# Optimization experiments

Measured on AMD Instinct MI355X. Metric: run time of the kernel, lower is better.

The kernel has to match this reference:

```python
import jax, jax.numpy as jnp
import numpy as np

D_MODEL = 1024
NUM_HEADS = 16
DEPTH = D_MODEL // NUM_HEADS


def setup_inputs() -> dict:
    key = jax.random.key(0)
    ks = jax.random.split(key, 6)
    B, S = 2, 2048
    scale = 1.0 / np.sqrt(D_MODEL)
    return {
        "q": jax.random.normal(ks[0], (B, S, D_MODEL), jnp.float32),
        "k": jax.random.normal(ks[1], (B, S, D_MODEL), jnp.float32),
        "v": jax.random.normal(ks[2], (B, S, D_MODEL), jnp.float32),
        "wq": jax.random.normal(ks[3], (D_MODEL, D_MODEL), jnp.float32) * scale,
        "wk": jax.random.normal(ks[4], (D_MODEL, D_MODEL), jnp.float32) * scale,
        "wv": jax.random.normal(ks[5], (D_MODEL, D_MODEL), jnp.float32) * scale,
    }


def reference(q, k, v, wq, wk, wv):
    B, S, _ = q.shape
    # Linear projections (nn.Linear: x @ W.T), then split heads -> [B,H,S,depth]
    def split(x):
        return x.reshape(B, -1, NUM_HEADS, DEPTH).transpose(0, 2, 1, 3)
    Q = split(q @ wq.T)
    K = split(k @ wk.T)
    V = split(v @ wv.T)
    scores = jnp.einsum("bhqd,bhkd->bhqk", Q, K) / np.sqrt(DEPTH).astype(np.float32)
    attn = jax.nn.softmax(scores, axis=-1)
    out = jnp.einsum("bhqk,bhkd->bhqd", attn, V)
    # merge heads; note: original forward never applies self.dense
    return out.transpose(0, 2, 1, 3).reshape(B, S, D_MODEL)
```

## Files before the change

kernel.cpp:

```cpp
#include <hip/hip_runtime.h>
#include <hip/hip_bf16.h>
#include <stdint.h>

#define B_SZ 2
#define S_LEN 2048
#define DM 1024
#define NH 16
#define DEPTH 64
#define M_ROWS (B_SZ * S_LEN)
#define SCALE_Q 0.1803368801111144f

typedef __attribute__((ext_vector_type(8))) short bf16x8;
typedef __attribute__((ext_vector_type(4))) float f32x4;
typedef __attribute__((ext_vector_type(16))) float f32x16;

__device__ __forceinline__ unsigned short f2bf(float x) {
    union { float f; unsigned u; } a; a.f = x;
    unsigned r = a.u + 0x7FFF + ((a.u >> 16) & 1);
    return (unsigned short)(r >> 16);
}

__device__ __forceinline__ bf16x8 u4_to_bf8(uint4 u) {
    union { uint4 a; bf16x8 b; } c; c.a = u; return c.b;
}

__device__ __forceinline__ unsigned cvtpk_bf16(float lo, float hi) {
    unsigned r;
    asm("v_cvt_pk_bf16_f32 %0, %1, %2" : "=v"(r) : "v"(lo), "v"(hi));
    return r;
}

__device__ __forceinline__ void permswap32(unsigned &a, unsigned &b) {
    auto r = __builtin_amdgcn_permlane32_swap(a, b, false, false);
    a = r[0]; b = r[1];
}

__device__ __forceinline__ void async_ld16(const unsigned short* g, void* l) {
    __builtin_amdgcn_global_load_lds(
        (const __attribute__((address_space(1))) void*)g,
        (__attribute__((address_space(3))) void*)l,
        16, 0, 0);
}


__global__ __launch_bounds__(256)
void convert_kernel(const float* __restrict__ q, const float* __restrict__ k,
                    const float* __restrict__ v, const float* __restrict__ wq,
                    const float* __restrict__ wk, const float* __restrict__ wv,
                    unsigned short* __restrict__ dst) {
    const int z = blockIdx.y;
    const float* src = (z == 0) ? q : (z == 1) ? k : (z == 2) ? v
                     : (z == 3) ? wq : (z == 4) ? wk : wv;
    const size_t n4  = (z < 3) ? ((size_t)M_ROWS * DM / 4) : ((size_t)DM * DM / 4);
    const size_t off = (z < 3) ? ((size_t)z * M_ROWS * DM)
                               : ((size_t)3 * M_ROWS * DM + (size_t)(z - 3) * DM * DM);
    unsigned short* d = dst + off;
    const size_t stride = (size_t)gridDim.x * blockDim.x;
    for (size_t i = (size_t)blockIdx.x * blockDim.x + threadIdx.x; i < n4; i += stride) {
        float4 x = ((const float4*)src)[i];
        ushort4 p;
        p.x = f2bf(x.x); p.y = f2bf(x.y); p.z = f2bf(x.z); p.w = f2bf(x.w);
        ((ushort4*)d)[i] = p;
    }
}

__global__ __launch_bounds__(256)
void proj_gemm3_kernel(const unsigned short* __restrict__ Xall,
                       const unsigned short* __restrict__ Wall,
                       unsigned short* __restrict__ Call) {
    __shared__ unsigned short As[128 * 64];
    __shared__ unsigned short Bs[128 * 64];

    const int z = blockIdx.z;
    const unsigned short* X = Xall + (size_t)z * M_ROWS * DM;
    const unsigned short* W = Wall + (size_t)z * DM * DM;
    unsigned short* C = Call + (size_t)z * M_ROWS * DM;

    const int tid  = threadIdx.x;
    const int wave = tid >> 6;
    const int lane = tid & 63;
    const int l32  = lane & 31;
    const int s    = lane >> 5;
    const int m0 = blockIdx.x * 128;
    const int n0 = blockIdx.y * 128;
    const int wm = (wave >> 1) * 64;
    const int wn = (wave & 1) * 64;

    const int r8 = lane >> 3;
    const int sc = (lane & 7) ^ r8;

    f32x16 acc[2][2];
#pragma unroll
    for (int mi = 0; mi < 2; ++mi)
#pragma unroll
        for (int ni = 0; ni < 2; ++ni)
#pragma unroll
            for (int r = 0; r < 16; ++r) acc[mi][ni][r] = 0.f;

    for (int k0 = 0; k0 < DM; k0 += 64) {
#pragma unroll
        for (int i = 0; i < 4; ++i) {
            const int r = i * 32 + wave * 8 + r8;
            async_ld16(X + (size_t)(m0 + r) * DM + k0 + sc * 8,
                       (char*)As + i * 4096 + wave * 1024);
            async_ld16(W + (size_t)(n0 + r) * DM + k0 + sc * 8,
                       (char*)Bs + i * 4096 + wave * 1024);
        }
        __syncthreads();

#pragma unroll
        for (int ch = 0; ch < 4; ++ch) {
            bf16x8 af[2], bfr[2];
#pragma unroll
            for (int mi = 0; mi < 2; ++mi) {
                const int row = wm + mi * 32 + l32;
                af[mi] = *(const bf16x8*)&As[row * 64 + (((2 * ch + s) ^ (row & 7)) * 8)];
            }
#pragma unroll
            for (int ni = 0; ni < 2; ++ni) {
                const int row = wn + ni * 32 + l32;
                bfr[ni] = *(const bf16x8*)&Bs[row * 64 + (((2 * ch + s) ^ (row & 7)) * 8)];
            }
#pragma unroll
            for (int mi = 0; mi < 2; ++mi)
#pragma unroll
                for (int ni = 0; ni < 2; ++ni)
                    acc[mi][ni] = __builtin_amdgcn_mfma_f32_32x32x16_bf16(
                        af[mi], bfr[ni], acc[mi][ni], 0, 0, 0);
        }
        __syncthreads();
    }

    const float scale = (z == 0) ? SCALE_Q : 1.0f;
#pragma unroll
    for (int mi = 0; mi < 2; ++mi)
#pragma unroll
        for (int ni = 0; ni < 2; ++ni)
#pragma unroll
            for (int r = 0; r < 16; ++r) {
                const int row = m0 + wm + mi * 32 + (r & 3) + 8 * (r >> 2) + 4 * s;
                const int col = n0 + wn + ni * 32 + l32;
                C[(size_t)row * DM + col] = f2bf(acc[mi][ni][r] * scale);
            }
}

__global__ __launch_bounds__(256)
void vtrans_kernel(const unsigned short* __restrict__ Vp,
                   unsigned short* __restrict__ Vt) {
    __shared__ unsigned short Ls[64 * 72];
    const int tr = blockIdx.x;
    const int h  = blockIdx.y;
    const int tid = threadIdx.x;

#pragma unroll
    for (int i = 0; i < 2; ++i) {
        const int id = i * 256 + tid;
        const int r = id >> 3, c = id & 7;
        bf16x8 v8 = *(const bf16x8*)&Vp[(size_t)(tr * 64 + r) * DM + h * 64 + c * 8];
        *(bf16x8*)&Ls[r * 72 + ((c ^ (r & 7)) * 8)] = v8;
    }
    __syncthreads();

    const int b = tr >> 5;
    const int col0 = (tr & 31) * 64;
#pragma unroll
    for (int i = 0; i < 2; ++i) {
        const int id = i * 256 + tid;
        const int d = id >> 3, c2 = id & 7;
        unsigned short tmp[8];
#pragma unroll
        for (int j = 0; j < 8; ++j) {
            const int t = c2 * 8 + j;
            tmp[j] = Ls[t * 72 + (((d >> 3) ^ (t & 7)) * 8) + (d & 7)];
        }
        *(bf16x8*)&Vt[(size_t)((b * NH + h) * DEPTH + d) * S_LEN + col0 + c2 * 8] =
            *(const bf16x8*)tmp;
    }
}

__global__ __launch_bounds__(128, 2)
void attn8_kernel(const unsigned short* __restrict__ Qp,
                  const unsigned short* __restrict__ Kp,
                  const unsigned short* __restrict__ Vt,
                  float* __restrict__ out,
                  float* __restrict__ Op1,
                  float* __restrict__ lp) {
    __shared__ __align__(16) char smem[32768];
    unsigned short* Ks = (unsigned short*)smem;
    unsigned short* Vs = (unsigned short*)(smem + 16384);

    const int tid  = threadIdx.x;
    const int w    = tid >> 6;
    const int lane = tid & 63;
    const int l32  = lane & 31;
    const int s    = lane >> 5;
    const int r8   = lane >> 3;
    const int sc   = (lane & 7) ^ r8;

    const int q0 = blockIdx.x * 128 + w * 64;
    const int h  = blockIdx.y;
    const int z  = blockIdx.z;
    const int b     = z >> 1;
    const int split = z & 1;
    const int tbase = split * 1024;

    const unsigned short* Kg = Kp + (size_t)(b * S_LEN + tbase) * DM + h * DEPTH;
    const unsigned short* Vg = Vt + (size_t)((b * NH + h) * DEPTH) * S_LEN + tbase;
    float* obase = split ? Op1 : out;
    float* lbase = lp + (size_t)split * M_ROWS * NH;

    bf16x8 qf[2][4];
#pragma unroll
    for (int nq = 0; nq < 2; ++nq) {
        const unsigned short* p =
            Qp + (size_t)(b * S_LEN + q0 + nq * 32 + l32) * DM + h * DEPTH;
#pragma unroll
        for (int ch = 0; ch < 4; ++ch)
            qf[nq][ch] = *(const bf16x8*)(p + ch * 16 + s * 8);
    }

    f32x16 oacc[2][2];
    float lacc[2] = {0.f, 0.f};
#pragma unroll
    for (int db = 0; db < 2; ++db)
#pragma unroll
        for (int nq = 0; nq < 2; ++nq)
#pragma unroll
            for (int r = 0; r < 16; ++r) oacc[db][nq][r] = 0.f;

#pragma unroll
    for (int i = 0; i < 4; ++i)
        async_ld16(Kg + (size_t)(w * 32 + i * 8 + r8) * DM + sc * 8,
                   (char*)smem + w * 4096 + i * 1024);
#pragma unroll
    for (int i = 0; i < 4; ++i)
        async_ld16(Vg + (size_t)(w * 32 + i * 8 + r8) * S_LEN + sc * 8,
                   (char*)smem + 16384 + w * 4096 + i * 1024);

    for (int it = 0; it < 16; ++it) {
        const int cb = it & 1;

        asm volatile("s_waitcnt vmcnt(0) lgkmcnt(0)" ::: "memory");
        __syncthreads();

        if (it < 15) {
            const int tn = (it + 1) * 64;
            char* kd = (char*)smem + (cb ^ 1) * 8192 + w * 4096;
            char* vd = (char*)smem + 16384 + (cb ^ 1) * 8192 + w * 4096;
#pragma unroll
            for (int i = 0; i < 4; ++i)
                async_ld16(Kg + (size_t)(tn + w * 32 + i * 8 + r8) * DM + sc * 8,
                           kd + i * 1024);
#pragma unroll
            for (int i = 0; i < 4; ++i)
                async_ld16(Vg + (size_t)(w * 32 + i * 8 + r8) * S_LEN + tn + sc * 8,
                           vd + i * 1024);
        }

        const unsigned short* Kb = Ks + cb * 4096;
        const unsigned short* Vb = Vs + cb * 4096;

#pragma unroll
        for (int th = 0; th < 2; ++th) {
            const unsigned short* Kh = Kb + th * 2048;
            const int vcb = th * 4;

            f32x16 s0, s1;
#pragma unroll
            for (int r = 0; r < 16; ++r) { s0[r] = 0.f; s1[r] = 0.f; }
            __builtin_amdgcn_s_setprio(1);
#pragma unroll
            for (int ch = 0; ch < 4; ++ch) {
                bf16x8 kf = *(const bf16x8*)
                    &Kh[l32 * 64 + (((2 * ch + s) ^ (l32 & 7)) * 8)];
                s0 = __builtin_amdgcn_mfma_f32_32x32x16_bf16(kf, qf[0][ch], s0, 0, 0, 0);
                s1 = __builtin_amdgcn_mfma_f32_32x32x16_bf16(kf, qf[1][ch], s1, 0, 0, 0);
            }
            __builtin_amdgcn_s_setprio(0);

            unsigned pw[2][8];
#pragma unroll
            for (int nq = 0; nq < 2; ++nq) {
                float p[16];
#pragma unroll
                for (int r = 0; r < 16; ++r)
                    p[r] = __builtin_amdgcn_exp2f(nq ? s1[r] : s0[r]);
                lacc[nq] += ((p[0] + p[1]) + (p[2] + p[3]))
                          + ((p[4] + p[5]) + (p[6] + p[7]))
                          + ((p[8] + p[9]) + (p[10] + p[11]))
                          + ((p[12] + p[13]) + (p[14] + p[15]));
                unsigned a0 = cvtpk_bf16(p[0],  p[1]);
                unsigned b0 = cvtpk_bf16(p[4],  p[5]);
                unsigned a1 = cvtpk_bf16(p[2],  p[3]);
                unsigned b1 = cvtpk_bf16(p[6],  p[7]);
                unsigned a2 = cvtpk_bf16(p[8],  p[9]);
                unsigned b2 = cvtpk_bf16(p[12], p[13]);
                unsigned a3 = cvtpk_bf16(p[10], p[11]);
                unsigned b3 = cvtpk_bf16(p[14], p[15]);
                permswap32(a0, b0);
                permswap32(a1, b1);
                permswap32(a2, b2);
                permswap32(a3, b3);
                pw[nq][0] = a0; pw[nq][1] = a1; pw[nq][2] = b0; pw[nq][3] = b1;
                pw[nq][4] = a2; pw[nq][5] = a3; pw[nq][6] = b2; pw[nq][7] = b3;
            }

#pragma unroll
            for (int ch = 0; ch < 2; ++ch) {
                bf16x8 pf[2];
#pragma unroll
                for (int nq = 0; nq < 2; ++nq) {
                    uint4 pu;
                    pu.x = pw[nq][ch * 4 + 0];
                    pu.y = pw[nq][ch * 4 + 1];
                    pu.z = pw[nq][ch * 4 + 2];
                    pu.w = pw[nq][ch * 4 + 3];
                    pf[nq] = u4_to_bf8(pu);
                }
                __builtin_amdgcn_s_setprio(1);
#pragma unroll
                for (int db = 0; db < 2; ++db) {
                    const int drow = db * 32 + l32;
                    bf16x8 vf = *(const bf16x8*)
                        &Vb[drow * 64 + (((vcb + 2 * ch + s) ^ (l32 & 7)) * 8)];
                    oacc[db][0] = __builtin_amdgcn_mfma_f32_32x32x16_bf16(
                        vf, pf[0], oacc[db][0], 0, 0, 0);
                    oacc[db][1] = __builtin_amdgcn_mfma_f32_32x32x16_bf16(
                        vf, pf[1], oacc[db][1], 0, 0, 0);
                }
                __builtin_amdgcn_s_setprio(0);
            }
        }
    }

    asm volatile("s_waitcnt vmcnt(0)" ::: "memory");

    const float l0 = lacc[0] + __shfl_xor(lacc[0], 32, 64);
    const float l1 = lacc[1] + __shfl_xor(lacc[1], 32, 64);
    if (s == 0) {
        lbase[(size_t)(b * S_LEN + q0 + l32) * NH + h]      = l0;
        lbase[(size_t)(b * S_LEN + q0 + 32 + l32) * NH + h] = l1;
    }

    __syncthreads();
    float* Of = (float*)(smem + w * 4608);
#pragma unroll
    for (int c = 0; c < 4; ++c) {
        const int nq = c >> 1;
        if ((l32 >> 4) == (c & 1)) {
            const int qh = l32 & 15;
#pragma unroll
            for (int db = 0; db < 2; ++db)
#pragma unroll
                for (int m = 0; m < 4; ++m) {
                    float4 v;
                    v.x = oacc[db][nq][4 * m + 0];
                    v.y = oacc[db][nq][4 * m + 1];
                    v.z = oacc[db][nq][4 * m + 2];
                    v.w = oacc[db][nq][4 * m + 3];
                    *(float4*)&Of[qh * 68 + db * 32 + 8 * m + 4 * s] = v;
                }
        }
        asm volatile("" ::: "memory");
#pragma unroll
        for (int i = 0; i < 4; ++i) {
            const int row = i * 4 + (lane >> 4);
            const int c4 = lane & 15;
            float4 v = *(const float4*)&Of[row * 68 + c4 * 4];
            *(float4*)&obase[(size_t)(b * S_LEN + q0 + c * 16 + row) * DM
                             + h * DEPTH + c4 * 4] = v;
        }
        asm volatile("" ::: "memory");
    }
}

__global__ __launch_bounds__(256)
void combine_kernel(float* __restrict__ out, const float* __restrict__ Op1,
                    const float* __restrict__ lp) {
    const int i4 = blockIdx.x * 256 + threadIdx.x;
    const int row = i4 >> 8;
    const int c4  = i4 & 255;
    const int h   = c4 >> 4;
    const float l = lp[row * NH + h] + lp[M_ROWS * NH + row * NH + h];
    const float inv = 1.0f / l;
    float4 a = ((const float4*)out)[i4];
    float4 bq = ((const float4*)Op1)[i4];
    a.x = (a.x + bq.x) * inv;
    a.y = (a.y + bq.y) * inv;
    a.z = (a.z + bq.z) * inv;
    a.w = (a.w + bq.w) * inv;
    ((float4*)out)[i4] = a;
}

#define LDK 72

__global__ __launch_bounds__(256)
void proj_gemm_kernel(const float* __restrict__ q, const float* __restrict__ k,
                      const float* __restrict__ v, const float* __restrict__ wq,
                      const float* __restrict__ wk, const float* __restrict__ wv,
                      unsigned short* __restrict__ Qp, unsigned short* __restrict__ Kp,
                      unsigned short* __restrict__ Vp) {
    __shared__ unsigned short As[128 * LDK];
    __shared__ unsigned short Bs[128 * LDK];

    const int z = blockIdx.z;
    const float* __restrict__ X = (z == 0) ? q : (z == 1) ? k : v;
    const float* __restrict__ W = (z == 0) ? wq : (z == 1) ? wk : wv;
    unsigned short* __restrict__ C = (z == 0) ? Qp : (z == 1) ? Kp : Vp;

    const int tid  = threadIdx.x;
    const int wave = tid >> 6;
    const int lane = tid & 63;
    const int quad = lane >> 4;
    const int l16  = lane & 15;
    const int m0 = blockIdx.x * 128;
    const int n0 = blockIdx.y * 128;
    const int wm = (wave >> 1) * 64;
    const int wn = (wave & 1) * 64;

    f32x4 acc[4][4];
#pragma unroll
    for (int mt = 0; mt < 4; ++mt)
#pragma unroll
        for (int nt = 0; nt < 4; ++nt)
            acc[mt][nt] = (f32x4){0.f, 0.f, 0.f, 0.f};

    for (int k0 = 0; k0 < DM; k0 += 64) {
#pragma unroll
        for (int vv = 0; vv < 8; ++vv) {
            int vecid = tid + 256 * vv;
            int r  = vecid >> 4;
            int c4 = vecid & 15;
            const float4 xa = *(const float4*)&X[(size_t)(m0 + r) * DM + k0 + c4 * 4];
            ushort4 pa;
            pa.x = f2bf(xa.x); pa.y = f2bf(xa.y); pa.z = f2bf(xa.z); pa.w = f2bf(xa.w);
            *(ushort4*)&As[r * LDK + c4 * 4] = pa;
            const float4 xb = *(const float4*)&W[(size_t)(n0 + r) * DM + k0 + c4 * 4];
            ushort4 pb;
            pb.x = f2bf(xb.x); pb.y = f2bf(xb.y); pb.z = f2bf(xb.z); pb.w = f2bf(xb.w);
            *(ushort4*)&Bs[r * LDK + c4 * 4] = pb;
        }
        __syncthreads();

#pragma unroll
        for (int kc = 0; kc < 2; ++kc) {
            bf16x8 af[4], bfr[4];
#pragma unroll
            for (int mt = 0; mt < 4; ++mt)
                af[mt] = *(const bf16x8*)&As[(wm + mt * 16 + l16) * LDK + kc * 32 + quad * 8];
#pragma unroll
            for (int nt = 0; nt < 4; ++nt)
                bfr[nt] = *(const bf16x8*)&Bs[(wn + nt * 16 + l16) * LDK + kc * 32 + quad * 8];
#pragma unroll
            for (int mt = 0; mt < 4; ++mt)
#pragma unroll
                for (int nt = 0; nt < 4; ++nt)
                    acc[mt][nt] = __builtin_amdgcn_mfma_f32_16x16x32_bf16(
                        af[mt], bfr[nt], acc[mt][nt], 0, 0, 0);
        }
        __syncthreads();
    }

#pragma unroll
    for (int mt = 0; mt < 4; ++mt)
#pragma unroll
        for (int nt = 0; nt < 4; ++nt)
#pragma unroll
            for (int r = 0; r < 4; ++r) {
                int row = m0 + wm + mt * 16 + quad * 4 + r;
                int col = n0 + wn + nt * 16 + l16;
                C[(size_t)row * DM + col] = f2bf(acc[mt][nt][r]);
            }
}

__global__ __launch_bounds__(256)
void attn_kernel(const unsigned short* __restrict__ Qp,
                 const unsigned short* __restrict__ Kp,
                 const unsigned short* __restrict__ Vp,
                 float* __restrict__ out) {
    __shared__ unsigned short Ks[64 * LDK];
    __shared__ unsigned short Vtl[64 * LDK];
    __shared__ unsigned short Ps[4 * 16 * LDK];

    const int tid  = threadIdx.x;
    const int wave = tid >> 6;
    const int lane = tid & 63;
    const int quad = lane >> 4;
    const int l16  = lane & 15;
    const int q0 = blockIdx.x * 64;
    const int h  = blockIdx.y;
    const int b  = blockIdx.z;
    const int wbase = wave * 16 * LDK;

    bf16x8 qf[2];
    {
        size_t row = (size_t)b * S_LEN + q0 + wave * 16 + l16;
        const unsigned short* p = Qp + row * DM + h * DEPTH;
        qf[0] = *(const bf16x8*)(p + quad * 8);
        qf[1] = *(const bf16x8*)(p + 32 + quad * 8);
    }

    float m_i[4], l_i[4];
    f32x4 accO[4];
#pragma unroll
    for (int r = 0; r < 4; ++r) { m_i[r] = -1e30f; l_i[r] = 0.f; }
#pragma unroll
    for (int f = 0; f < 4; ++f) accO[f] = (f32x4){0.f, 0.f, 0.f, 0.f};

    for (int t0 = 0; t0 < S_LEN; t0 += 64) {
#pragma unroll
        for (int vv = 0; vv < 2; ++vv) {
            int vecid = tid + 256 * vv;
            int r  = vecid >> 3;
            int cv = vecid & 7;
            size_t grow = (size_t)(b * S_LEN + t0 + r) * DM + h * DEPTH + cv * 8;
            *(bf16x8*)&Ks[r * LDK + cv * 8] = *(const bf16x8*)(Kp + grow);
            bf16x8 vvv = *(const bf16x8*)(Vp + grow);
#pragma unroll
            for (int j = 0; j < 8; ++j)
                Vtl[(cv * 8 + j) * LDK + r] = ((const unsigned short*)&vvv)[j];
        }
        __syncthreads();

        f32x4 sc4[4];
#pragma unroll
        for (int nt = 0; nt < 4; ++nt) {
            f32x4 a = (f32x4){0.f, 0.f, 0.f, 0.f};
            bf16x8 kf0 = *(const bf16x8*)&Ks[(nt * 16 + l16) * LDK + quad * 8];
            bf16x8 kf1 = *(const bf16x8*)&Ks[(nt * 16 + l16) * LDK + 32 + quad * 8];
            a = __builtin_amdgcn_mfma_f32_16x16x32_bf16(qf[0], kf0, a, 0, 0, 0);
            a = __builtin_amdgcn_mfma_f32_16x16x32_bf16(qf[1], kf1, a, 0, 0, 0);
            sc4[nt] = a;
        }
#pragma unroll
        for (int nt = 0; nt < 4; ++nt)
#pragma unroll
            for (int r = 0; r < 4; ++r) sc4[nt][r] *= 0.125f;

#pragma unroll
        for (int r = 0; r < 4; ++r) {
            float mx = fmaxf(fmaxf(sc4[0][r], sc4[1][r]), fmaxf(sc4[2][r], sc4[3][r]));
#pragma unroll
            for (int off = 1; off < 16; off <<= 1)
                mx = fmaxf(mx, __shfl_xor(mx, off, 64));
            float mnew = fmaxf(m_i[r], mx);
            float alpha = __expf(m_i[r] - mnew);
            float rs = 0.f;
#pragma unroll
            for (int nt = 0; nt < 4; ++nt) {
                float p = __expf(sc4[nt][r] - mnew);
                sc4[nt][r] = p;
                rs += p;
            }
#pragma unroll
            for (int off = 1; off < 16; off <<= 1)
                rs += __shfl_xor(rs, off, 64);
            l_i[r] = l_i[r] * alpha + rs;
            m_i[r] = mnew;
#pragma unroll
            for (int f = 0; f < 4; ++f) accO[f][r] *= alpha;
        }

#pragma unroll
        for (int nt = 0; nt < 4; ++nt)
#pragma unroll
            for (int r = 0; r < 4; ++r)
                Ps[wbase + (quad * 4 + r) * LDK + nt * 16 + l16] = f2bf(sc4[nt][r]);
        __syncthreads();

        bf16x8 pf0 = *(const bf16x8*)&Ps[wbase + l16 * LDK + quad * 8];
        bf16x8 pf1 = *(const bf16x8*)&Ps[wbase + l16 * LDK + 32 + quad * 8];
#pragma unroll
        for (int f = 0; f < 4; ++f) {
            bf16x8 vf0 = *(const bf16x8*)&Vtl[(f * 16 + l16) * LDK + quad * 8];
            bf16x8 vf1 = *(const bf16x8*)&Vtl[(f * 16 + l16) * LDK + 32 + quad * 8];
            accO[f] = __builtin_amdgcn_mfma_f32_16x16x32_bf16(pf0, vf0, accO[f], 0, 0, 0);
            accO[f] = __builtin_amdgcn_mfma_f32_16x16x32_bf16(pf1, vf1, accO[f], 0, 0, 0);
        }
        __syncthreads();
    }

#pragma unroll
    for (int f = 0; f < 4; ++f)
#pragma unroll
        for (int r = 0; r < 4; ++r) {
            size_t row = (size_t)b * S_LEN + q0 + wave * 16 + quad * 4 + r;
            out[row * DM + h * DEPTH + f * 16 + l16] = accO[f][r] / l_i[r];
        }
}

extern "C" void kernel_launch(void* const* d_in, const int* in_sizes, int n_in,
                              void* d_out, int out_size, void* d_ws, size_t ws_size,
                              hipStream_t stream) {
    const float* q  = (const float*)d_in[0];
    const float* k  = (const float*)d_in[1];
    const float* v  = (const float*)d_in[2];
    const float* wq = (const float*)d_in[3];
    const float* wk = (const float*)d_in[4];
    const float* wv = (const float*)d_in[5];
    float* out = (float*)d_out;

    unsigned short* ws = (unsigned short*)d_ws;
    const size_t NPROJ = (size_t)M_ROWS * DM;
    const size_t NW    = (size_t)DM * DM;

    const size_t need = (3 * NPROJ + 3 * NW + 3 * NPROJ) * sizeof(unsigned short);

    if (ws_size >= need) {
        unsigned short* Xbf = ws;
        unsigned short* Wbf = ws + 3 * NPROJ;
        unsigned short* Cp  = ws + 3 * NPROJ + 3 * NW;
        unsigned short* Qp  = Cp;
        unsigned short* Kp  = Cp + NPROJ;
        unsigned short* Vp  = Cp + 2 * NPROJ;
        unsigned short* Vt  = ws;
        float*          Op1 = (float*)(ws + NPROJ);
        float*          lp  = (float*)(ws + 3 * NPROJ);

        convert_kernel<<<dim3(256, 6), 256, 0, stream>>>(q, k, v, wq, wk, wv, Xbf);
        proj_gemm3_kernel<<<dim3(M_ROWS / 128, DM / 128, 3), 256, 0, stream>>>(Xbf, Wbf, Cp);
        vtrans_kernel<<<dim3(M_ROWS / 64, NH), 256, 0, stream>>>(Vp, Vt);
        attn8_kernel<<<dim3(S_LEN / 128, NH, 4), 128, 0, stream>>>(
            Qp, Kp, Vt, out, Op1, lp);
        combine_kernel<<<dim3(M_ROWS * DM / 4 / 256), 256, 0, stream>>>(out, Op1, lp);
    } else {
        unsigned short* Qp = ws;
        unsigned short* Kp = ws + NPROJ;
        unsigned short* Vp = ws + 2 * NPROJ;
        proj_gemm_kernel<<<dim3(M_ROWS / 128, DM / 128, 3), 256, 0, stream>>>(
            q, k, v, wq, wk, wv, Qp, Kp, Vp);
        attn_kernel<<<dim3(S_LEN / 64, NH, B_SZ), 256, 0, stream>>>(Qp, Kp, Vp, out);
    }
}
```

Baseline: 198.1 us.

## Load K/V fragments directly from global into registers, dropping LDS staging

Replaces the shared-memory double-buffered async K/V tile pipeline in the attention kernel with per-wave direct global loads into register fragments. Loads for the next 32-key half-tile are issued before the current half-step computes. This removes the block barriers and LDS traffic, and shrinks shared memory to only the output staging buffer. The cost is that each wave now fetches K and V separately, so global and L2 traffic roughly doubles. The reads are also narrower, 16B per lane on strided rows, and register pressure rises.

```diff
diff --git a/kernel.cpp b/kernel.cpp
--- a/kernel.cpp
+++ b/kernel.cpp
@@ -178,6 +178,85 @@
     }
 }
 
+__device__ __forceinline__ void attn_half_step(
+    const bf16x8* kf, const bf16x8* vf, const bf16x8 (&qf)[2][4],
+    f32x16 (&oacc)[2][2], float* lacc) {
+    f32x16 s0, s1;
+#pragma unroll
+    for (int r = 0; r < 16; ++r) { s0[r] = 0.f; s1[r] = 0.f; }
+    __builtin_amdgcn_s_setprio(1);
+#pragma unroll
+    for (int ch = 0; ch < 4; ++ch) {
+        s0 = __builtin_amdgcn_mfma_f32_32x32x16_bf16(kf[ch], qf[0][ch], s0, 0, 0, 0);
+        s1 = __builtin_amdgcn_mfma_f32_32x32x16_bf16(kf[ch], qf[1][ch], s1, 0, 0, 0);
+    }
+    __builtin_amdgcn_s_setprio(0);
+
+    unsigned pw[2][8];
+#pragma unroll
+    for (int nq = 0; nq < 2; ++nq) {
+        float p[16];
+#pragma unroll
+        for (int r = 0; r < 16; ++r)
+            p[r] = __builtin_amdgcn_exp2f(nq ? s1[r] : s0[r]);
+        lacc[nq] += ((p[0] + p[1]) + (p[2] + p[3]))
+                  + ((p[4] + p[5]) + (p[6] + p[7]))
+                  + ((p[8] + p[9]) + (p[10] + p[11]))
+                  + ((p[12] + p[13]) + (p[14] + p[15]));
+        unsigned a0 = cvtpk_bf16(p[0],  p[1]);
+        unsigned b0 = cvtpk_bf16(p[4],  p[5]);
+        unsigned a1 = cvtpk_bf16(p[2],  p[3]);
+        unsigned b1 = cvtpk_bf16(p[6],  p[7]);
+        unsigned a2 = cvtpk_bf16(p[8],  p[9]);
+        unsigned b2 = cvtpk_bf16(p[12], p[13]);
+        unsigned a3 = cvtpk_bf16(p[10], p[11]);
+        unsigned b3 = cvtpk_bf16(p[14], p[15]);
+        permswap32(a0, b0);
+        permswap32(a1, b1);
+        permswap32(a2, b2);
+        permswap32(a3, b3);
+        pw[nq][0] = a0; pw[nq][1] = a1; pw[nq][2] = b0; pw[nq][3] = b1;
+        pw[nq][4] = a2; pw[nq][5] = a3; pw[nq][6] = b2; pw[nq][7] = b3;
+    }
+
+#pragma unroll
+    for (int ch = 0; ch < 2; ++ch) {
+        bf16x8 pf[2];
+#pragma unroll
+        for (int nq = 0; nq < 2; ++nq) {
+            uint4 pu;
+            pu.x = pw[nq][ch * 4 + 0];
+            pu.y = pw[nq][ch * 4 + 1];
+            pu.z = pw[nq][ch * 4 + 2];
+            pu.w = pw[nq][ch * 4 + 3];
+            pf[nq] = u4_to_bf8(pu);
+        }
+        __builtin_amdgcn_s_setprio(1);
+#pragma unroll
+        for (int db = 0; db < 2; ++db) {
+            oacc[db][0] = __builtin_amdgcn_mfma_f32_32x32x16_bf16(
+                vf[ch * 2 + db], pf[0], oacc[db][0], 0, 0, 0);
+            oacc[db][1] = __builtin_amdgcn_mfma_f32_32x32x16_bf16(
+                vf[ch * 2 + db], pf[1], oacc[db][1], 0, 0, 0);
+        }
+        __builtin_amdgcn_s_setprio(0);
+    }
+}
+
+__device__ __forceinline__ void load_kf(bf16x8* kf, const unsigned short* kp) {
+#pragma unroll
+    for (int ch = 0; ch < 4; ++ch)
+        kf[ch] = *(const bf16x8*)(kp + ch * 16);
+}
+__device__ __forceinline__ void load_vf(bf16x8* vf, const unsigned short* vp0,
+                                        const unsigned short* vp1) {
+#pragma unroll
+    for (int ch = 0; ch < 2; ++ch) {
+        vf[ch * 2 + 0] = *(const bf16x8*)(vp0 + ch * 16);
+        vf[ch * 2 + 1] = *(const bf16x8*)(vp1 + ch * 16);
+    }
+}
+
 __global__ __launch_bounds__(128, 2)
 void attn8_kernel(const unsigned short* __restrict__ Qp,
                   const unsigned short* __restrict__ Kp,
@@ -185,17 +264,13 @@
                   float* __restrict__ out,
                   float* __restrict__ Op1,
                   float* __restrict__ lp) {
-    __shared__ __align__(16) char smem[32768];
-    unsigned short* Ks = (unsigned short*)smem;
-    unsigned short* Vs = (unsigned short*)(smem + 16384);
+    __shared__ __align__(16) float Of_s[2][1088];
 
     const int tid  = threadIdx.x;
     const int w    = tid >> 6;
     const int lane = tid & 63;
     const int l32  = lane & 31;
     const int s    = lane >> 5;
-    const int r8   = lane >> 3;
-    const int sc   = (lane & 7) ^ r8;
 
     const int q0 = blockIdx.x * 128 + w * 64;
     const int h  = blockIdx.y;
@@ -228,112 +303,27 @@
 #pragma unroll
             for (int r = 0; r < 16; ++r) oacc[db][nq][r] = 0.f;
 
-#pragma unroll
-    for (int i = 0; i < 4; ++i)
-        async_ld16(Kg + (size_t)(w * 32 + i * 8 + r8) * DM + sc * 8,
-                   (char*)smem + w * 4096 + i * 1024);
-#pragma unroll
-    for (int i = 0; i < 4; ++i)
-        async_ld16(Vg + (size_t)(w * 32 + i * 8 + r8) * S_LEN + sc * 8,
-                   (char*)smem + 16384 + w * 4096 + i * 1024);
-
-    for (int it = 0; it < 16; ++it) {
-        const int cb = it & 1;
-
-        asm volatile("s_waitcnt vmcnt(0) lgkmcnt(0)" ::: "memory");
-        __syncthreads();
-
-        if (it < 15) {
-            const int tn = (it + 1) * 64;
-            char* kd = (char*)smem + (cb ^ 1) * 8192 + w * 4096;
-            char* vd = (char*)smem + 16384 + (cb ^ 1) * 8192 + w * 4096;
-#pragma unroll
-            for (int i = 0; i < 4; ++i)
-                async_ld16(Kg + (size_t)(tn + w * 32 + i * 8 + r8) * DM + sc * 8,
-                           kd + i * 1024);
-#pragma unroll
-            for (int i = 0; i < 4; ++i)
-                async_ld16(Vg + (size_t)(w * 32 + i * 8 + r8) * S_LEN + tn + sc * 8,
-                           vd + i * 1024);
-        }
-
-        const unsigned short* Kb = Ks + cb * 4096;
-        const unsigned short* Vb = Vs + cb * 4096;
-
-#pragma unroll
-        for (int th = 0; th < 2; ++th) {
-            const unsigned short* Kh = Kb + th * 2048;
-            const int vcb = th * 4;
-
-            f32x16 s0, s1;
-#pragma unroll
-            for (int r = 0; r < 16; ++r) { s0[r] = 0.f; s1[r] = 0.f; }
-            __builtin_amdgcn_s_setprio(1);
-#pragma unroll
-            for (int ch = 0; ch < 4; ++ch) {
-                bf16x8 kf = *(const bf16x8*)
-                    &Kh[l32 * 64 + (((2 * ch + s) ^ (l32 & 7)) * 8)];
-                s0 = __builtin_amdgcn_mfma_f32_32x32x16_bf16(kf, qf[0][ch], s0, 0, 0, 0);
-                s1 = __builtin_amdgcn_mfma_f32_32x32x16_bf16(kf, qf[1][ch], s1, 0, 0, 0);
-            }
-            __builtin_amdgcn_s_setprio(0);
-
-            unsigned pw[2][8];
-#pragma unroll
-            for (int nq = 0; nq < 2; ++nq) {
-                float p[16];
-#pragma unroll
-                for (int r = 0; r < 16; ++r)
-                    p[r] = __builtin_amdgcn_exp2f(nq ? s1[r] : s0[r]);
-                lacc[nq] += ((p[0] + p[1]) + (p[2] + p[3]))
-                          + ((p[4] + p[5]) + (p[6] + p[7]))
-                          + ((p[8] + p[9]) + (p[10] + p[11]))
-                          + ((p[12] + p[13]) + (p[14] + p[15]));
-                unsigned a0 = cvtpk_bf16(p[0],  p[1]);
-                unsigned b0 = cvtpk_bf16(p[4],  p[5]);
-                unsigned a1 = cvtpk_bf16(p[2],  p[3]);
-                unsigned b1 = cvtpk_bf16(p[6],  p[7]);
-                unsigned a2 = cvtpk_bf16(p[8],  p[9]);
-                unsigned b2 = cvtpk_bf16(p[12], p[13]);
-                unsigned a3 = cvtpk_bf16(p[10], p[11]);
-                unsigned b3 = cvtpk_bf16(p[14], p[15]);
-                permswap32(a0, b0);
-                permswap32(a1, b1);
-                permswap32(a2, b2);
-                permswap32(a3, b3);
-                pw[nq][0] = a0; pw[nq][1] = a1; pw[nq][2] = b0; pw[nq][3] = b1;
-                pw[nq][4] = a2; pw[nq][5] = a3; pw[nq][6] = b2; pw[nq][7] = b3;
-            }
-
-#pragma unroll
-            for (int ch = 0; ch < 2; ++ch) {
-                bf16x8 pf[2];
-#pragma unroll
-                for (int nq = 0; nq < 2; ++nq) {
-                    uint4 pu;
-                    pu.x = pw[nq][ch * 4 + 0];
-                    pu.y = pw[nq][ch * 4 + 1];
-                    pu.z = pw[nq][ch * 4 + 2];
-                    pu.w = pw[nq][ch * 4 + 3];
-                    pf[nq] = u4_to_bf8(pu);
-                }
-                __builtin_amdgcn_s_setprio(1);
-#pragma unroll
-                for (int db = 0; db < 2; ++db) {
-                    const int drow = db * 32 + l32;
-                    bf16x8 vf = *(const bf16x8*)
-                        &Vb[drow * 64 + (((vcb + 2 * ch + s) ^ (l32 & 7)) * 8)];
-                    oacc[db][0] = __builtin_amdgcn_mfma_f32_32x32x16_bf16(
-                        vf, pf[0], oacc[db][0], 0, 0, 0);
-                    oacc[db][1] = __builtin_amdgcn_mfma_f32_32x32x16_bf16(
-                        vf, pf[1], oacc[db][1], 0, 0, 0);
-                }
-                __builtin_amdgcn_s_setprio(0);
-            }
-        }
-    }
-
-    asm volatile("s_waitcnt vmcnt(0)" ::: "memory");
+    const unsigned short* kp  = Kg + (size_t)l32 * DM + s * 8;
+    const unsigned short* vp0 = Vg + (size_t)l32 * S_LEN + s * 8;
+    const unsigned short* vp1 = Vg + (size_t)(32 + l32) * S_LEN + s * 8;
+
+    bf16x8 kA[4], vA[4], kB[4], vB[4];
+    load_kf(kA, kp);
+    load_vf(vA, vp0, vp1);
+
+    for (int hp = 0; hp < 16; ++hp) {
+        load_kf(kB, kp + 32 * DM);
+        load_vf(vB, vp0 + 32, vp1 + 32);
+        attn_half_step(kA, vA, qf, oacc, lacc);
+        if (hp < 15) {
+            load_kf(kA, kp + 64 * DM);
+            load_vf(vA, vp0 + 64, vp1 + 64);
+        }
+        attn_half_step(kB, vB, qf, oacc, lacc);
+        kp  += 64 * DM;
+        vp0 += 64;
+        vp1 += 64;
+    }
 
     const float l0 = lacc[0] + __shfl_xor(lacc[0], 32, 64);
     const float l1 = lacc[1] + __shfl_xor(lacc[1], 32, 64);
@@ -342,8 +332,7 @@
         lbase[(size_t)(b * S_LEN + q0 + 32 + l32) * NH + h] = l1;
     }
 
-    __syncthreads();
-    float* Of = (float*)(smem + w * 4608);
+    float* Of = Of_s[w];
 #pragma unroll
     for (int c = 0; c < 4; ++c) {
         const int nq = c >> 1;
```

Result: slower. 213.2 us (+7.6%).

## Split attention block across four waves with 32 query rows each

Applied to the files above, without the earlier changes.

The attention kernel now runs 256 threads (four waves) per block instead of two. Each wave handles 32 query rows instead of 64, and the K/V tile loads are spread across four waves. This cuts per-wave register use (one score accumulator and two output accumulators) so more waves can be resident. In exchange, each K/V fragment read from shared memory feeds fewer MFMAs, which lowers data reuse per wave.

```diff
diff --git a/kernel.cpp b/kernel.cpp
--- a/kernel.cpp
+++ b/kernel.cpp
@@ -178,7 +178,7 @@
     }
 }
 
-__global__ __launch_bounds__(128, 2)
+__global__ __launch_bounds__(256, 4)
 void attn8_kernel(const unsigned short* __restrict__ Qp,
                   const unsigned short* __restrict__ Kp,
                   const unsigned short* __restrict__ Vt,
@@ -197,7 +197,7 @@
     const int r8   = lane >> 3;
     const int sc   = (lane & 7) ^ r8;
 
-    const int q0 = blockIdx.x * 128 + w * 64;
+    const int q0 = blockIdx.x * 128 + w * 32;
     const int h  = blockIdx.y;
     const int z  = blockIdx.z;
     const int b     = z >> 1;
@@ -209,33 +209,29 @@
     float* obase = split ? Op1 : out;
     float* lbase = lp + (size_t)split * M_ROWS * NH;
 
-    bf16x8 qf[2][4];
-#pragma unroll
-    for (int nq = 0; nq < 2; ++nq) {
+    bf16x8 qf[4];
+    {
         const unsigned short* p =
-            Qp + (size_t)(b * S_LEN + q0 + nq * 32 + l32) * DM + h * DEPTH;
+            Qp + (size_t)(b * S_LEN + q0 + l32) * DM + h * DEPTH;
 #pragma unroll
         for (int ch = 0; ch < 4; ++ch)
-            qf[nq][ch] = *(const bf16x8*)(p + ch * 16 + s * 8);
-    }
-
-    f32x16 oacc[2][2];
-    float lacc[2] = {0.f, 0.f};
+            qf[ch] = *(const bf16x8*)(p + ch * 16 + s * 8);
+    }
+
+    f32x16 oacc[2];
+    float lacc = 0.f;
 #pragma unroll
     for (int db = 0; db < 2; ++db)
 #pragma unroll
-        for (int nq = 0; nq < 2; ++nq)
-#pragma unroll
-            for (int r = 0; r < 16; ++r) oacc[db][nq][r] = 0.f;
-
-#pragma unroll
-    for (int i = 0; i < 4; ++i)
-        async_ld16(Kg + (size_t)(w * 32 + i * 8 + r8) * DM + sc * 8,
-                   (char*)smem + w * 4096 + i * 1024);
-#pragma unroll
-    for (int i = 0; i < 4; ++i)
-        async_ld16(Vg + (size_t)(w * 32 + i * 8 + r8) * S_LEN + sc * 8,
-                   (char*)smem + 16384 + w * 4096 + i * 1024);
+        for (int r = 0; r < 16; ++r) oacc[db][r] = 0.f;
+
+#pragma unroll
+    for (int i = 0; i < 2; ++i) {
+        async_ld16(Kg + (size_t)(w * 16 + i * 8 + r8) * DM + sc * 8,
+                   (char*)smem + w * 2048 + i * 1024);
+        async_ld16(Vg + (size_t)(w * 16 + i * 8 + r8) * S_LEN + sc * 8,
+                   (char*)smem + 16384 + w * 2048 + i * 1024);
+    }
 
     for (int it = 0; it < 16; ++it) {
         const int cb = it & 1;
@@ -245,16 +241,15 @@
 
         if (it < 15) {
             const int tn = (it + 1) * 64;
-            char* kd = (char*)smem + (cb ^ 1) * 8192 + w * 4096;
-            char* vd = (char*)smem + 16384 + (cb ^ 1) * 8192 + w * 4096;
-#pragma unroll
-            for (int i = 0; i < 4; ++i)
-                async_ld16(Kg + (size_t)(tn + w * 32 + i * 8 + r8) * DM + sc * 8,
+            char* kd = (char*)smem + (cb ^ 1) * 8192 + w * 2048;
+            char* vd = (char*)smem + 16384 + (cb ^ 1) * 8192 + w * 2048;
+#pragma unroll
+            for (int i = 0; i < 2; ++i) {
+                async_ld16(Kg + (size_t)(tn + w * 16 + i * 8 + r8) * DM + sc * 8,
                            kd + i * 1024);
-#pragma unroll
-            for (int i = 0; i < 4; ++i)
-                async_ld16(Vg + (size_t)(w * 32 + i * 8 + r8) * S_LEN + tn + sc * 8,
+                async_ld16(Vg + (size_t)(w * 16 + i * 8 + r8) * S_LEN + tn + sc * 8,
                            vd + i * 1024);
+            }
         }
 
         const unsigned short* Kb = Ks + cb * 4096;
@@ -265,68 +260,58 @@
             const unsigned short* Kh = Kb + th * 2048;
             const int vcb = th * 4;
 
-            f32x16 s0, s1;
-#pragma unroll
-            for (int r = 0; r < 16; ++r) { s0[r] = 0.f; s1[r] = 0.f; }
+            f32x16 s0;
+#pragma unroll
+            for (int r = 0; r < 16; ++r) s0[r] = 0.f;
             __builtin_amdgcn_s_setprio(1);
 #pragma unroll
             for (int ch = 0; ch < 4; ++ch) {
                 bf16x8 kf = *(const bf16x8*)
                     &Kh[l32 * 64 + (((2 * ch + s) ^ (l32 & 7)) * 8)];
-                s0 = __builtin_amdgcn_mfma_f32_32x32x16_bf16(kf, qf[0][ch], s0, 0, 0, 0);
-                s1 = __builtin_amdgcn_mfma_f32_32x32x16_bf16(kf, qf[1][ch], s1, 0, 0, 0);
+                s0 = __builtin_amdgcn_mfma_f32_32x32x16_bf16(kf, qf[ch], s0, 0, 0, 0);
             }
             __builtin_amdgcn_s_setprio(0);
 
-            unsigned pw[2][8];
-#pragma unroll
-            for (int nq = 0; nq < 2; ++nq) {
-                float p[16];
-#pragma unroll
-                for (int r = 0; r < 16; ++r)
-                    p[r] = __builtin_amdgcn_exp2f(nq ? s1[r] : s0[r]);
-                lacc[nq] += ((p[0] + p[1]) + (p[2] + p[3]))
-                          + ((p[4] + p[5]) + (p[6] + p[7]))
-                          + ((p[8] + p[9]) + (p[10] + p[11]))
-                          + ((p[12] + p[13]) + (p[14] + p[15]));
-                unsigned a0 = cvtpk_bf16(p[0],  p[1]);
-                unsigned b0 = cvtpk_bf16(p[4],  p[5]);
-                unsigned a1 = cvtpk_bf16(p[2],  p[3]);
-                unsigned b1 = cvtpk_bf16(p[6],  p[7]);
-                unsigned a2 = cvtpk_bf16(p[8],  p[9]);
-                unsigned b2 = cvtpk_bf16(p[12], p[13]);
-                unsigned a3 = cvtpk_bf16(p[10], p[11]);
-                unsigned b3 = cvtpk_bf16(p[14], p[15]);
-                permswap32(a0, b0);
-                permswap32(a1, b1);
-                permswap32(a2, b2);
-                permswap32(a3, b3);
-                pw[nq][0] = a0; pw[nq][1] = a1; pw[nq][2] = b0; pw[nq][3] = b1;
-                pw[nq][4] = a2; pw[nq][5] = a3; pw[nq][6] = b2; pw[nq][7] = b3;
-            }
+            float p[16];
+#pragma unroll
+            for (int r = 0; r < 16; ++r)
+                p[r] = __builtin_amdgcn_exp2f(s0[r]);
+            lacc += ((p[0] + p[1]) + (p[2] + p[3]))
+                  + ((p[4] + p[5]) + (p[6] + p[7]))
+                  + ((p[8] + p[9]) + (p[10] + p[11]))
+                  + ((p[12] + p[13]) + (p[14] + p[15]));
+            unsigned a0 = cvtpk_bf16(p[0],  p[1]);
+            unsigned b0 = cvtpk_bf16(p[4],  p[5]);
+            unsigned a1 = cvtpk_bf16(p[2],  p[3]);
+            unsigned b1 = cvtpk_bf16(p[6],  p[7]);
+            unsigned a2 = cvtpk_bf16(p[8],  p[9]);
+            unsigned b2 = cvtpk_bf16(p[12], p[13]);
+            unsigned a3 = cvtpk_bf16(p[10], p[11]);
+            unsigned b3 = cvtpk_bf16(p[14], p[15]);
+            permswap32(a0, b0);
+            permswap32(a1, b1);
+            permswap32(a2, b2);
+            permswap32(a3, b3);
+            unsigned pw[8];
+            pw[0] = a0; pw[1] = a1; pw[2] = b0; pw[3] = b1;
+            pw[4] = a2; pw[5] = a3; pw[6] = b2; pw[7] = b3;
 
 #pragma unroll
             for (int ch = 0; ch < 2; ++ch) {
-                bf16x8 pf[2];
-#pragma unroll
-                for (int nq = 0; nq < 2; ++nq) {
-                    uint4 pu;
-                    pu.x = pw[nq][ch * 4 + 0];
-                    pu.y = pw[nq][ch * 4 + 1];
-                    pu.z = pw[nq][ch * 4 + 2];
-                    pu.w = pw[nq][ch * 4 + 3];
-                    pf[nq] = u4_to_bf8(pu);
-                }
+                uint4 pu;
+                pu.x = pw[ch * 4 + 0];
+                pu.y = pw[ch * 4 + 1];
+                pu.z = pw[ch * 4 + 2];
+                pu.w = pw[ch * 4 + 3];
+                bf16x8 pf = u4_to_bf8(pu);
                 __builtin_amdgcn_s_setprio(1);
 #pragma unroll
                 for (int db = 0; db < 2; ++db) {
                     const int drow = db * 32 + l32;
                     bf16x8 vf = *(const bf16x8*)
                         &Vb[drow * 64 + (((vcb + 2 * ch + s) ^ (l32 & 7)) * 8)];
-                    oacc[db][0] = __builtin_amdgcn_mfma_f32_32x32x16_bf16(
-                        vf, pf[0], oacc[db][0], 0, 0, 0);
-                    oacc[db][1] = __builtin_amdgcn_mfma_f32_32x32x16_bf16(
-                        vf, pf[1], oacc[db][1], 0, 0, 0);
+                    oacc[db] = __builtin_amdgcn_mfma_f32_32x32x16_bf16(
+                        vf, pf, oacc[db], 0, 0, 0);
                 }
                 __builtin_amdgcn_s_setprio(0);
             }
@@ -335,29 +320,25 @@
 
     asm volatile("s_waitcnt vmcnt(0)" ::: "memory");
 
-    const float l0 = lacc[0] + __shfl_xor(lacc[0], 32, 64);
-    const float l1 = lacc[1] + __shfl_xor(lacc[1], 32, 64);
-    if (s == 0) {
-        lbase[(size_t)(b * S_LEN + q0 + l32) * NH + h]      = l0;
-        lbase[(size_t)(b * S_LEN + q0 + 32 + l32) * NH + h] = l1;
-    }
+    const float l0 = lacc + __shfl_xor(lacc, 32, 64);
+    if (s == 0)
+        lbase[(size_t)(b * S_LEN + q0 + l32) * NH + h] = l0;
 
     __syncthreads();
     float* Of = (float*)(smem + w * 4608);
 #pragma unroll
-    for (int c = 0; c < 4; ++c) {
-        const int nq = c >> 1;
-        if ((l32 >> 4) == (c & 1)) {
+    for (int c = 0; c < 2; ++c) {
+        if ((l32 >> 4) == c) {
             const int qh = l32 & 15;
 #pragma unroll
             for (int db = 0; db < 2; ++db)
 #pragma unroll
                 for (int m = 0; m < 4; ++m) {
                     float4 v;
-                    v.x = oacc[db][nq][4 * m + 0];
-                    v.y = oacc[db][nq][4 * m + 1];
-                    v.z = oacc[db][nq][4 * m + 2];
-                    v.w = oacc[db][nq][4 * m + 3];
+                    v.x = oacc[db][4 * m + 0];
+                    v.y = oacc[db][4 * m + 1];
+                    v.z = oacc[db][4 * m + 2];
+                    v.w = oacc[db][4 * m + 3];
                     *(float4*)&Of[qh * 68 + db * 32 + 8 * m + 4 * s] = v;
                 }
         }
@@ -620,7 +601,7 @@
         convert_kernel<<<dim3(256, 6), 256, 0, stream>>>(q, k, v, wq, wk, wv, Xbf);
         proj_gemm3_kernel<<<dim3(M_ROWS / 128, DM / 128, 3), 256, 0, stream>>>(Xbf, Wbf, Cp);
         vtrans_kernel<<<dim3(M_ROWS / 64, NH), 256, 0, stream>>>(Vp, Vt);
-        attn8_kernel<<<dim3(S_LEN / 128, NH, 4), 128, 0, stream>>>(
+        attn8_kernel<<<dim3(S_LEN / 128, NH, 4), 256, 0, stream>>>(
             Qp, Kp, Vt, out, Op1, lp);
         combine_kernel<<<dim3(M_ROWS * DM / 4 / 256), 256, 0, stream>>>(out, Op1, lp);
     } else {
```

Measured after the change: 198.8 us. No clear change (+0.3%).
